# Kernel tuning notes

Hardware: AMD Instinct MI355X
Metric: run time of the kernel (lower is better)

## Reference

```python
import jax, jax.numpy as jnp
import numpy as np

N_NODES = 100000
N_EDGES = 1600000
IN_FEATS = 256
DIMS = [IN_FEATS, 128, 64, 16, 40]


def setup_inputs() -> dict:
    key = jax.random.key(0)
    ks = jax.random.split(key, 3 + 2 * 4)
    x = jax.random.normal(ks[0], (N_NODES, IN_FEATS), dtype=jnp.float32)
    src = jax.random.randint(ks[1], (N_EDGES,), 0, N_NODES)
    dst = jax.random.randint(ks[2], (N_EDGES,), 0, N_NODES)
    inp = {"x": x, "src": src, "dst": dst}
    for i in range(4):
        fan_in = DIMS[i]
        inp[f"W{i+1}"] = jax.random.normal(ks[3 + 2 * i], (DIMS[i], DIMS[i + 1]), dtype=jnp.float32) / np.sqrt(fan_in)
        inp[f"b{i+1}"] = jnp.zeros((DIMS[i + 1],), dtype=jnp.float32)
    return inp


def reference(x, src, dst, W1, b1, W2, b2, W3, b3, W4, b4):
    n = x.shape[0]
    ones = jnp.ones(src.shape[0], dtype=x.dtype)
    # symmetric GCN normalization (DGL norm='both'); clamp deg>=1 like DGL
    deg_out = jnp.maximum(jax.ops.segment_sum(ones, src, num_segments=n), 1.0)
    deg_in = jnp.maximum(jax.ops.segment_sum(ones, dst, num_segments=n), 1.0)
    norm_src = jax.lax.rsqrt(deg_out)[:, None]  # [N,1]
    norm_dst = jax.lax.rsqrt(deg_in)[:, None]   # [N,1]

    def gconv(h, W, b, act):
        # project first (in_feats >= out_feats for every layer, matching DGL ordering)
        h = (h * norm_src) @ W                                   # [N, d_out]
        h = jax.ops.segment_sum(h[src], dst, num_segments=n)      # SpMM aggregate
        h = h * norm_dst + b
        return jax.nn.relu(h) if act else h

    h = gconv(x, W1, b1, True)
    h = gconv(h, W2, b2, True)
    h = gconv(h, W3, b3, True)
    h = gconv(h, W4, b4, False)
    return h
```

## Files before the change

### kernel.cpp

```cpp
#include <hip/hip_runtime.h>


typedef unsigned short ushort_t;

__device__ __forceinline__ void gload_lds16(const float4* g, float4* l) {
    __builtin_amdgcn_global_load_lds(
        (const __attribute__((address_space(1))) void*)g,
        (__attribute__((address_space(3))) void*)l, 16, 0, 0);
}

__device__ __forceinline__ ushort_t f2bf(float f) {
    unsigned u = __float_as_uint(f);
    u += 0x7FFFu + ((u >> 16) & 1u);
    return (ushort_t)(u >> 16);
}
#define BFLO(u) __uint_as_float((u) << 16)
#define BFHI(u) __uint_as_float((u) & 0xffff0000u)

template<int DIN, int DOUT, int RB, int KT, typename EPI>
__device__ __forceinline__ void proj_body(
        const float* __restrict__ in, const float* __restrict__ W,
        int N, int n0, float4* __restrict__ wlds, float4* __restrict__ xlds,
        EPI&& epi) {
    constexpr int CG  = DOUT / 4;
    constexpr int RPP = 256 / CG;
    constexpr int R4  = RB / RPP;
    constexpr int K4T = KT / 4;
    constexpr int NKT = DIN / KT;
    constexpr int XTILE = RB * K4T;
    constexpr int WTILE = KT * CG;
    static_assert(RPP * CG == 256, "full block");
    static_assert((K4T & (K4T - 1)) == 0, "pow2 swizzle");
    static_assert(XTILE % 256 == 0 && WTILE % 256 == 0, "stage granularity");

    const int tid  = threadIdx.x;
    const int wave = tid >> 6;
    const int lane = tid & 63;
    const int rp   = tid / CG;
    const int cg   = tid - rp * CG;

    float4 acc[R4];
#pragma unroll
    for (int r = 0; r < R4; ++r) acc[r] = make_float4(0.f, 0.f, 0.f, 0.f);

    for (int kt = 0; kt < NKT; ++kt) {
        const float4* wsrc = (const float4*)(W + (size_t)kt * KT * DOUT);
#pragma unroll
        for (int j = 0; j < WTILE / 256; ++j) {
            int base = j * 256 + wave * 64;
            gload_lds16(wsrc + base + lane, &wlds[base]);
        }
#pragma unroll
        for (int j = 0; j < XTILE / 256; ++j) {
            int base = j * 256 + wave * 64;
            int fi   = base + lane;
            int row  = fi / K4T;
            int k4   = fi - row * K4T;
            int k4s  = k4 ^ (row & (K4T - 1));
            int grow = n0 + row; if (grow >= N) grow = N - 1;
            const float4* gsrc = (const float4*)(in + (size_t)grow * DIN) + kt * K4T + k4s;
            gload_lds16(gsrc, &xlds[base]);
        }
        __syncthreads();
#pragma unroll 2
        for (int k4 = 0; k4 < K4T; ++k4) {
            float4 w0 = wlds[(k4 * 4 + 0) * CG + cg];
            float4 w1 = wlds[(k4 * 4 + 1) * CG + cg];
            float4 w2 = wlds[(k4 * 4 + 2) * CG + cg];
            float4 w3 = wlds[(k4 * 4 + 3) * CG + cg];
#pragma unroll
            for (int r = 0; r < R4; ++r) {
                int row = rp + r * RPP;
                float4 xv = xlds[row * K4T + (k4 ^ (row & (K4T - 1)))];
                acc[r].x = fmaf(xv.x, w0.x, acc[r].x);
                acc[r].y = fmaf(xv.x, w0.y, acc[r].y);
                acc[r].z = fmaf(xv.x, w0.z, acc[r].z);
                acc[r].w = fmaf(xv.x, w0.w, acc[r].w);
                acc[r].x = fmaf(xv.y, w1.x, acc[r].x);
                acc[r].y = fmaf(xv.y, w1.y, acc[r].y);
                acc[r].z = fmaf(xv.y, w1.z, acc[r].z);
                acc[r].w = fmaf(xv.y, w1.w, acc[r].w);
                acc[r].x = fmaf(xv.z, w2.x, acc[r].x);
                acc[r].y = fmaf(xv.z, w2.y, acc[r].y);
                acc[r].z = fmaf(xv.z, w2.z, acc[r].z);
                acc[r].w = fmaf(xv.z, w2.w, acc[r].w);
                acc[r].x = fmaf(xv.w, w3.x, acc[r].x);
                acc[r].y = fmaf(xv.w, w3.y, acc[r].y);
                acc[r].z = fmaf(xv.w, w3.z, acc[r].z);
                acc[r].w = fmaf(xv.w, w3.w, acc[r].w);
            }
        }
        __syncthreads();
    }
    epi(acc, rp, cg);
}

template<int DIN, int DOUT, int RB, int KT>
__global__ void __launch_bounds__(256) k_comb(
        const float* __restrict__ x, const float* __restrict__ W,
        ushort_t* __restrict__ outbf, int N,
        const int* __restrict__ src, const int* __restrict__ dst,
        int* __restrict__ degO, int* __restrict__ degI,
        int* __restrict__ rank, int E, int PB, int HTH) {
    constexpr int CG  = DOUT / 4;
    constexpr int RPP = 256 / CG;
    constexpr int R4  = RB / RPP;
    constexpr int K4T = KT / 4;
    __shared__ float4 wlds[KT * CG];
    __shared__ float4 xlds[RB * K4T];

    int bid = blockIdx.x, g = bid / 5, r = bid - g * 5;
    if (r == 4) {
        int H = HTH;
        int i = g * 256 + (int)threadIdx.x;
        for (; i + 3 * H < E; i += 4 * H) {
            int s0 = src[i],         d0 = dst[i];
            int s1 = src[i + H],     d1 = dst[i + H];
            int s2 = src[i + 2 * H], d2 = dst[i + 2 * H];
            int s3 = src[i + 3 * H], d3 = dst[i + 3 * H];
            atomicAdd(&degO[s0], 1); atomicAdd(&degO[s1], 1);
            atomicAdd(&degO[s2], 1); atomicAdd(&degO[s3], 1);
            int r0 = atomicAdd(&degI[d0], 1);
            int r1 = atomicAdd(&degI[d1], 1);
            int r2 = atomicAdd(&degI[d2], 1);
            int r3 = atomicAdd(&degI[d3], 1);
            rank[i] = r0; rank[i + H] = r1;
            rank[i + 2 * H] = r2; rank[i + 3 * H] = r3;
        }
        for (; i < E; i += H) {
            atomicAdd(&degO[src[i]], 1);
            rank[i] = atomicAdd(&degI[dst[i]], 1);
        }
        return;
    }
    int pidx = g * 4 + r;
    if (pidx >= PB) return;
    int n0 = pidx * RB;
    proj_body<DIN, DOUT, RB, KT>(x, W, N, n0, wlds, xlds,
        [&](float4 (&acc)[R4], int rp, int cg) {
#pragma unroll
            for (int rr = 0; rr < R4; ++rr) {
                int n = n0 + rp + rr * RPP;
                if (n < N) {
                    ushort4 s;
                    s.x = f2bf(acc[rr].x); s.y = f2bf(acc[rr].y);
                    s.z = f2bf(acc[rr].z); s.w = f2bf(acc[rr].w);
                    *(ushort4*)(outbf + (size_t)n * DOUT + cg * 4) = s;
                }
            }
        });
}

template<int DIN, int DOUT, int RB, int KT>
__global__ void __launch_bounds__(256) k_proj_gl2b(
        const float* __restrict__ in, const float* __restrict__ nrm,
        const float* __restrict__ W, ushort_t* __restrict__ outbf, int N) {
    constexpr int CG  = DOUT / 4;
    constexpr int RPP = 256 / CG;
    constexpr int R4  = RB / RPP;
    constexpr int K4T = KT / 4;
    __shared__ float4 wlds[KT * CG];
    __shared__ float4 xlds[RB * K4T];
    int n0 = blockIdx.x * RB;
    proj_body<DIN, DOUT, RB, KT>(in, W, N, n0, wlds, xlds,
        [&](float4 (&acc)[R4], int rp, int cg) {
#pragma unroll
            for (int rr = 0; rr < R4; ++rr) {
                int n = n0 + rp + rr * RPP;
                if (n < N) {
                    float nm = nrm[n];
                    ushort4 s;
                    s.x = f2bf(acc[rr].x * nm); s.y = f2bf(acc[rr].y * nm);
                    s.z = f2bf(acc[rr].z * nm); s.w = f2bf(acc[rr].w * nm);
                    *(ushort4*)(outbf + (size_t)n * DOUT + cg * 4) = s;
                }
            }
        });
}

__global__ void k_blocksum(const int* __restrict__ degI, const int* __restrict__ degO,
                           int* __restrict__ bsum, float* __restrict__ nSf,
                           float* __restrict__ nDf, int N) {
    __shared__ int sh[256];
    int base = blockIdx.x * 1024;
    int s = 0;
    for (int i = threadIdx.x; i < 1024; i += 256) {
        int idx = base + i;
        if (idx < N) {
            int d = degI[idx];
            s += d;
            nDf[idx] = rsqrtf((float)(d > 1 ? d : 1));
            int a = degO[idx];
            nSf[idx] = rsqrtf((float)(a > 1 ? a : 1));
        }
    }
    sh[threadIdx.x] = s; __syncthreads();
    for (int off = 128; off > 0; off >>= 1) {
        if (threadIdx.x < off) sh[threadIdx.x] += sh[threadIdx.x + off];
        __syncthreads();
    }
    if (threadIdx.x == 0) bsum[blockIdx.x] = sh[0];
}

__global__ void k_blockscan(const int* __restrict__ deg, const int* __restrict__ bsum,
                            int* __restrict__ rowptr, int N, int nb) {
    __shared__ int sh[256];
    int t = threadIdx.x;
    sh[t] = (t < nb) ? bsum[t] : 0;
    __syncthreads();
    for (int off = 1; off < 256; off <<= 1) {
        int v = (t >= off) ? sh[t - off] : 0;
        __syncthreads();
        sh[t] += v;
        __syncthreads();
    }
    int boff = (blockIdx.x > 0) ? sh[blockIdx.x - 1] : 0;
    __syncthreads();
    int base = blockIdx.x * 1024;
    int i0 = base + t * 4;
    int v[4]; int tot = 0;
#pragma unroll
    for (int r = 0; r < 4; ++r) {
        int idx = i0 + r;
        v[r] = (idx < N) ? deg[idx] : 0;
        tot += v[r];
    }
    sh[t] = tot; __syncthreads();
    for (int off = 1; off < 256; off <<= 1) {
        int x = (t >= off) ? sh[t - off] : 0;
        __syncthreads();
        sh[t] += x;
        __syncthreads();
    }
    int run = sh[t] - tot + boff;
#pragma unroll
    for (int r = 0; r < 4; ++r) {
        int idx = i0 + r;
        if (idx < N) rowptr[idx] = run;
        run += v[r];
    }
}

__global__ void k_fill3(const int* __restrict__ src, const int* __restrict__ dst,
                        const int* __restrict__ rank, const int* __restrict__ rowptr,
                        int* __restrict__ col, int E) {
    int stride = gridDim.x * blockDim.x;
    for (int i = blockIdx.x * blockDim.x + threadIdx.x; i < E; i += stride) {
        col[rowptr[dst[i]] + rank[i]] = src[i];
    }
}

__global__ void __launch_bounds__(256) k_gather_l1(
        const int* __restrict__ rowptr, const int* __restrict__ col,
        const int* __restrict__ degI, const float* __restrict__ nSf,
        const float* __restrict__ nDf, const ushort_t* __restrict__ projbf,
        const float* __restrict__ bias, float* __restrict__ out, int N) {
    constexpr int DOUT = 128;
    constexpr int CGB = DOUT / 8;
    long t = blockIdx.x * 256L + threadIdx.x;
    if (t >= (long)N * CGB) return;
    int n  = (int)(t / CGB);
    int cb = (int)(t - (long)n * CGB);
    int beg = rowptr[n];
    int dg  = degI[n];
    float acc[8];
#pragma unroll
    for (int k = 0; k < 8; ++k) acc[k] = 0.f;
    int i = 0;
    for (; i + 4 <= dg; i += 4) {
        int s0 = col[beg + i],     s1 = col[beg + i + 1];
        int s2 = col[beg + i + 2], s3 = col[beg + i + 3];
        uint4 v0 = *(const uint4*)(projbf + (size_t)s0 * DOUT + cb * 8);
        uint4 v1 = *(const uint4*)(projbf + (size_t)s1 * DOUT + cb * 8);
        uint4 v2 = *(const uint4*)(projbf + (size_t)s2 * DOUT + cb * 8);
        uint4 v3 = *(const uint4*)(projbf + (size_t)s3 * DOUT + cb * 8);
        float n0 = nSf[s0], n1 = nSf[s1], n2 = nSf[s2], n3 = nSf[s3];
        acc[0] = fmaf(n0, BFLO(v0.x), fmaf(n1, BFLO(v1.x), fmaf(n2, BFLO(v2.x), fmaf(n3, BFLO(v3.x), acc[0]))));
        acc[1] = fmaf(n0, BFHI(v0.x), fmaf(n1, BFHI(v1.x), fmaf(n2, BFHI(v2.x), fmaf(n3, BFHI(v3.x), acc[1]))));
        acc[2] = fmaf(n0, BFLO(v0.y), fmaf(n1, BFLO(v1.y), fmaf(n2, BFLO(v2.y), fmaf(n3, BFLO(v3.y), acc[2]))));
        acc[3] = fmaf(n0, BFHI(v0.y), fmaf(n1, BFHI(v1.y), fmaf(n2, BFHI(v2.y), fmaf(n3, BFHI(v3.y), acc[3]))));
        acc[4] = fmaf(n0, BFLO(v0.z), fmaf(n1, BFLO(v1.z), fmaf(n2, BFLO(v2.z), fmaf(n3, BFLO(v3.z), acc[4]))));
        acc[5] = fmaf(n0, BFHI(v0.z), fmaf(n1, BFHI(v1.z), fmaf(n2, BFHI(v2.z), fmaf(n3, BFHI(v3.z), acc[5]))));
        acc[6] = fmaf(n0, BFLO(v0.w), fmaf(n1, BFLO(v1.w), fmaf(n2, BFLO(v2.w), fmaf(n3, BFLO(v3.w), acc[6]))));
        acc[7] = fmaf(n0, BFHI(v0.w), fmaf(n1, BFHI(v1.w), fmaf(n2, BFHI(v2.w), fmaf(n3, BFHI(v3.w), acc[7]))));
    }
    for (; i < dg; ++i) {
        int s0 = col[beg + i];
        uint4 v0 = *(const uint4*)(projbf + (size_t)s0 * DOUT + cb * 8);
        float ns0 = nSf[s0];
        acc[0] = fmaf(ns0, BFLO(v0.x), acc[0]);
        acc[1] = fmaf(ns0, BFHI(v0.x), acc[1]);
        acc[2] = fmaf(ns0, BFLO(v0.y), acc[2]);
        acc[3] = fmaf(ns0, BFHI(v0.y), acc[3]);
        acc[4] = fmaf(ns0, BFLO(v0.z), acc[4]);
        acc[5] = fmaf(ns0, BFHI(v0.z), acc[5]);
        acc[6] = fmaf(ns0, BFLO(v0.w), acc[6]);
        acc[7] = fmaf(ns0, BFHI(v0.w), acc[7]);
    }
    float nm = nDf[n];
    const float* bp = bias + cb * 8;
    float o[8];
#pragma unroll
    for (int k = 0; k < 8; ++k) o[k] = fmaxf(fmaf(acc[k], nm, bp[k]), 0.f);
    float* dstp = out + (size_t)n * DOUT + cb * 8;
    *(float4*)(dstp)     = make_float4(o[0], o[1], o[2], o[3]);
    *(float4*)(dstp + 4) = make_float4(o[4], o[5], o[6], o[7]);
}

__global__ void __launch_bounds__(256) k_gather_fuse2(
        const int* __restrict__ rowptr, const int* __restrict__ col,
        const int* __restrict__ degI, const float* __restrict__ nSf,
        const float* __restrict__ nDf, const ushort_t* __restrict__ p2bf,
        const float* __restrict__ b2, const float* __restrict__ W3,
        float* __restrict__ P3, int N) {
    constexpr int DOUT = 64;
    __shared__ float w3s[64 * 16];
    ((float4*)w3s)[threadIdx.x] = ((const float4*)W3)[threadIdx.x];
    __syncthreads();

    long t = blockIdx.x * 256L + threadIdx.x;
    int n = (int)(t >> 3);
    bool valid = n < N;
    if (!valid) n = N - 1;
    int cb = (int)(t & 7);
    int lane = threadIdx.x & 63;
    int gb = lane & ~7;

    int beg = rowptr[n];
    int dg  = degI[n];
    float acc[8];
#pragma unroll
    for (int k = 0; k < 8; ++k) acc[k] = 0.f;
    int i = 0;
    for (; i + 4 <= dg; i += 4) {
        int s0 = col[beg + i],     s1 = col[beg + i + 1];
        int s2 = col[beg + i + 2], s3 = col[beg + i + 3];
        uint4 v0 = *(const uint4*)(p2bf + (size_t)s0 * DOUT + cb * 8);
        uint4 v1 = *(const uint4*)(p2bf + (size_t)s1 * DOUT + cb * 8);
        uint4 v2 = *(const uint4*)(p2bf + (size_t)s2 * DOUT + cb * 8);
        uint4 v3 = *(const uint4*)(p2bf + (size_t)s3 * DOUT + cb * 8);
        acc[0] += BFLO(v0.x) + BFLO(v1.x) + BFLO(v2.x) + BFLO(v3.x);
        acc[1] += BFHI(v0.x) + BFHI(v1.x) + BFHI(v2.x) + BFHI(v3.x);
        acc[2] += BFLO(v0.y) + BFLO(v1.y) + BFLO(v2.y) + BFLO(v3.y);
        acc[3] += BFHI(v0.y) + BFHI(v1.y) + BFHI(v2.y) + BFHI(v3.y);
        acc[4] += BFLO(v0.z) + BFLO(v1.z) + BFLO(v2.z) + BFLO(v3.z);
        acc[5] += BFHI(v0.z) + BFHI(v1.z) + BFHI(v2.z) + BFHI(v3.z);
        acc[6] += BFLO(v0.w) + BFLO(v1.w) + BFLO(v2.w) + BFLO(v3.w);
        acc[7] += BFHI(v0.w) + BFHI(v1.w) + BFHI(v2.w) + BFHI(v3.w);
    }
    for (; i < dg; ++i) {
        int s0 = col[beg + i];
        uint4 v0 = *(const uint4*)(p2bf + (size_t)s0 * DOUT + cb * 8);
        acc[0] += BFLO(v0.x); acc[1] += BFHI(v0.x);
        acc[2] += BFLO(v0.y); acc[3] += BFHI(v0.y);
        acc[4] += BFLO(v0.z); acc[5] += BFHI(v0.z);
        acc[6] += BFLO(v0.w); acc[7] += BFHI(v0.w);
    }
    float nm = nDf[n];
    float ns = nSf[n];
    const float* bp = b2 + cb * 8;
    float o[8];
#pragma unroll
    for (int k = 0; k < 8; ++k)
        o[k] = fmaxf(fmaf(acc[k], nm, bp[k]), 0.f) * ns;
    float y0 = 0.f, y1 = 0.f;
#pragma unroll
    for (int k = 0; k < 64; ++k) {
        float v = __shfl(o[k & 7], gb + (k >> 3), 64);
        y0 = fmaf(v, w3s[k * 16 + 2 * cb], y0);
        y1 = fmaf(v, w3s[k * 16 + 2 * cb + 1], y1);
    }
    if (valid) *(float2*)(P3 + (size_t)n * 16 + 2 * cb) = make_float2(y0, y1);
}

__global__ void __launch_bounds__(256) k_gather_l3(
        const int* __restrict__ rowptr, const int* __restrict__ col,
        const int* __restrict__ degI, const float* __restrict__ nSf,
        const float* __restrict__ nDf, const float* __restrict__ proj,
        const float* __restrict__ bias, float* __restrict__ out, int N) {
    long t = blockIdx.x * 256L + threadIdx.x;
    if (t >= (long)N * 4) return;
    int n  = (int)(t >> 2);
    int cg = (int)(t & 3);
    int beg = rowptr[n];
    int dg  = degI[n];
    float4 a0 = make_float4(0.f, 0.f, 0.f, 0.f);
    float4 a1 = make_float4(0.f, 0.f, 0.f, 0.f);
    float4 a2 = make_float4(0.f, 0.f, 0.f, 0.f);
    float4 a3 = make_float4(0.f, 0.f, 0.f, 0.f);
    int i = 0;
    for (; i + 4 <= dg; i += 4) {
        int s0 = col[beg + i],     s1 = col[beg + i + 1];
        int s2 = col[beg + i + 2], s3 = col[beg + i + 3];
        float4 v0 = *(const float4*)(proj + (size_t)s0 * 16 + cg * 4);
        float4 v1 = *(const float4*)(proj + (size_t)s1 * 16 + cg * 4);
        float4 v2 = *(const float4*)(proj + (size_t)s2 * 16 + cg * 4);
        float4 v3 = *(const float4*)(proj + (size_t)s3 * 16 + cg * 4);
        a0.x += v0.x; a0.y += v0.y; a0.z += v0.z; a0.w += v0.w;
        a1.x += v1.x; a1.y += v1.y; a1.z += v1.z; a1.w += v1.w;
        a2.x += v2.x; a2.y += v2.y; a2.z += v2.z; a2.w += v2.w;
        a3.x += v3.x; a3.y += v3.y; a3.z += v3.z; a3.w += v3.w;
    }
    for (; i < dg; ++i) {
        int s0 = col[beg + i];
        float4 v0 = *(const float4*)(proj + (size_t)s0 * 16 + cg * 4);
        a0.x += v0.x; a0.y += v0.y; a0.z += v0.z; a0.w += v0.w;
    }
    float4 s = make_float4(a0.x + a1.x + a2.x + a3.x, a0.y + a1.y + a2.y + a3.y,
                           a0.z + a1.z + a2.z + a3.z, a0.w + a1.w + a2.w + a3.w);
    float nm = nDf[n];
    float ns = nSf[n];
    float4 b = *(const float4*)(bias + cg * 4);
    float4 o;
    o.x = fmaxf(fmaf(s.x, nm, b.x), 0.f) * ns;
    o.y = fmaxf(fmaf(s.y, nm, b.y), 0.f) * ns;
    o.z = fmaxf(fmaf(s.z, nm, b.z), 0.f) * ns;
    o.w = fmaxf(fmaf(s.w, nm, b.w), 0.f) * ns;
    *(float4*)(out + (size_t)n * 16 + cg * 4) = o;
}

__global__ void __launch_bounds__(256) k_gather_fuse4(
        const int* __restrict__ rowptr, const int* __restrict__ col,
        const int* __restrict__ degI, const float* __restrict__ nDf,
        const float* __restrict__ t4, const float* __restrict__ W4,
        const float* __restrict__ b4, float* __restrict__ out, int N) {
    __shared__ float w4s[16 * 40];
    __shared__ float b4s[40];
    for (int i = threadIdx.x; i < 160; i += 256)
        ((float4*)w4s)[i] = ((const float4*)W4)[i];
    if (threadIdx.x < 40) b4s[threadIdx.x] = b4[threadIdx.x];
    __syncthreads();

    long t = blockIdx.x * 256L + threadIdx.x;
    int n = (int)(t >> 2);
    bool valid = n < N;
    if (!valid) n = N - 1;
    int cg = (int)(t & 3);
    int lane = threadIdx.x & 63;
    int gb = lane & ~3;

    int beg = rowptr[n];
    int dg  = degI[n];
    float4 a0 = make_float4(0.f, 0.f, 0.f, 0.f);
    float4 a1 = make_float4(0.f, 0.f, 0.f, 0.f);
    int i = 0;
    for (; i + 2 <= dg; i += 2) {
        int s0 = col[beg + i], s1 = col[beg + i + 1];
        float4 v0 = *(const float4*)(t4 + (size_t)s0 * 16 + cg * 4);
        float4 v1 = *(const float4*)(t4 + (size_t)s1 * 16 + cg * 4);
        a0.x += v0.x; a0.y += v0.y; a0.z += v0.z; a0.w += v0.w;
        a1.x += v1.x; a1.y += v1.y; a1.z += v1.z; a1.w += v1.w;
    }
    if (i < dg) {
        int s0 = col[beg + i];
        float4 v0 = *(const float4*)(t4 + (size_t)s0 * 16 + cg * 4);
        a0.x += v0.x; a0.y += v0.y; a0.z += v0.z; a0.w += v0.w;
    }
    float av[4] = { a0.x + a1.x, a0.y + a1.y, a0.z + a1.z, a0.w + a1.w };

    float y[10];
#pragma unroll
    for (int jj = 0; jj < 10; ++jj) y[jj] = 0.f;
#pragma unroll
    for (int k = 0; k < 16; ++k) {
        float v = __shfl(av[k & 3], gb + (k >> 2), 64);
        const float* wr = w4s + k * 40 + cg * 10;
#pragma unroll
        for (int jj = 0; jj < 10; ++jj) y[jj] = fmaf(v, wr[jj], y[jj]);
    }
    if (valid) {
        float nm = nDf[n];
        float* dp = out + (size_t)n * 40 + cg * 10;
        const float* bp = b4s + cg * 10;
#pragma unroll
        for (int jj = 0; jj < 10; ++jj) dp[jj] = fmaf(y[jj], nm, bp[jj]);
    }
}

static inline int cdiv(long a, int b) { return (int)((a + b - 1) / b); }

extern "C" void kernel_launch(void* const* d_in, const int* in_sizes, int n_in,
                              void* d_out, int out_size, void* d_ws, size_t ws_size,
                              hipStream_t stream) {
    const float* x   = (const float*)d_in[0];
    const int*   src = (const int*)d_in[1];
    const int*   dst = (const int*)d_in[2];
    const float* W1 = (const float*)d_in[3];  const float* b1 = (const float*)d_in[4];
    const float* W2 = (const float*)d_in[5];  const float* b2 = (const float*)d_in[6];
    const float* W3 = (const float*)d_in[7];  const float* b3 = (const float*)d_in[8];
    const float* W4 = (const float*)d_in[9];  const float* b4 = (const float*)d_in[10];

    const int N = in_sizes[0] / 256;
    const int E = in_sizes[1];

    int* ws_i = (int*)d_ws;
    int* degO   = ws_i;
    int* degI   = ws_i + N;
    int* rowptr = ws_i + 2 * (size_t)N;
    int* col    = ws_i + 3 * (size_t)N;
    int* rank   = ws_i + 3 * (size_t)N + E;
    float* nSf  = (float*)(ws_i + 3 * (size_t)N + 2 * (size_t)E);
    float* nDf  = nSf + N;
    float* projb = nDf + N;
    float* hbuf  = projb + (size_t)N * 64;
    ushort_t* projbf = (ushort_t*)projb;
    float* P3 = projb + (size_t)N * 32;
    int* bsum   = (int*)hbuf;

    int nb = (N + 1023) / 1024;
    int PB = cdiv(N, 64);
    int G5 = cdiv(PB, 4);
    int HTH = G5 * 256;

    hipMemsetAsync(degO, 0, 2 * (size_t)N * sizeof(int), stream);
    k_comb<256, 128, 64, 32><<<5 * G5, 256, 0, stream>>>(
        x, W1, projbf, N, src, dst, degO, degI, rank, E, PB, HTH);

    k_blocksum<<<nb, 256, 0, stream>>>(degI, degO, bsum, nSf, nDf, N);
    k_blockscan<<<nb, 256, 0, stream>>>(degI, bsum, rowptr, N, nb);
    k_fill3<<<2048, 256, 0, stream>>>(src, dst, rank, rowptr, col, E);

    k_gather_l1<<<cdiv((long)N * 16, 256), 256, 0, stream>>>(
        rowptr, col, degI, nSf, nDf, projbf, b1, hbuf, N);

    k_proj_gl2b<128, 64, 64, 32><<<cdiv(N, 64), 256, 0, stream>>>(
        hbuf, nSf, W2, projbf, N);
    k_gather_fuse2<<<cdiv((long)N * 8, 256), 256, 0, stream>>>(
        rowptr, col, degI, nSf, nDf, projbf, b2, W3, P3, N);

    k_gather_l3<<<cdiv((long)N * 4, 256), 256, 0, stream>>>(
        rowptr, col, degI, nSf, nDf, P3, b3, hbuf, N);

    k_gather_fuse4<<<cdiv((long)N * 4, 256), 256, 0, stream>>>(
        rowptr, col, degI, nDf, hbuf, W4, b4, (float*)d_out, N);
}
```

Measured before the change: 380.3 us.

## Store layer-1 activations as bf16 and add bf16-input layer-2 projection kernel

The layer-1 gather now writes its ReLU output as packed bf16 instead of fp32. A new dedicated layer-2 projection kernel reads those bf16 rows through a swizzled LDS tile and unpacks them before the FMA loop. This halves the bytes written and re-read for the intermediate activation, at the cost of extra precision loss in layer-1 outputs. The degree/rank atomic loop in the combined kernel is also simplified to a plain strided loop without the 4x manual unroll.

```diff
diff --git a/kernel.cpp b/kernel.cpp
--- a/kernel.cpp
+++ b/kernel.cpp
@@ -13,6 +13,9 @@
     unsigned u = __float_as_uint(f);
     u += 0x7FFFu + ((u >> 16) & 1u);
     return (ushort_t)(u >> 16);
+}
+__device__ __forceinline__ unsigned pack2bf(float a, float b) {
+    return (unsigned)f2bf(a) | ((unsigned)f2bf(b) << 16);
 }
 #define BFLO(u) __uint_as_float((u) << 16)
 #define BFHI(u) __uint_as_float((u) & 0xffff0000u)
@@ -111,23 +114,8 @@
 
     int bid = blockIdx.x, g = bid / 5, r = bid - g * 5;
     if (r == 4) {
-        int H = HTH;
         int i = g * 256 + (int)threadIdx.x;
-        for (; i + 3 * H < E; i += 4 * H) {
-            int s0 = src[i],         d0 = dst[i];
-            int s1 = src[i + H],     d1 = dst[i + H];
-            int s2 = src[i + 2 * H], d2 = dst[i + 2 * H];
-            int s3 = src[i + 3 * H], d3 = dst[i + 3 * H];
-            atomicAdd(&degO[s0], 1); atomicAdd(&degO[s1], 1);
-            atomicAdd(&degO[s2], 1); atomicAdd(&degO[s3], 1);
-            int r0 = atomicAdd(&degI[d0], 1);
-            int r1 = atomicAdd(&degI[d1], 1);
-            int r2 = atomicAdd(&degI[d2], 1);
-            int r3 = atomicAdd(&degI[d3], 1);
-            rank[i] = r0; rank[i + H] = r1;
-            rank[i + 2 * H] = r2; rank[i + 3 * H] = r3;
-        }
-        for (; i < E; i += H) {
+        for (; i < E; i += HTH) {
             atomicAdd(&degO[src[i]], 1);
             rank[i] = atomicAdd(&degI[dst[i]], 1);
         }
@@ -151,31 +139,64 @@
         });
 }
 
-template<int DIN, int DOUT, int RB, int KT>
-__global__ void __launch_bounds__(256) k_proj_gl2b(
-        const float* __restrict__ in, const float* __restrict__ nrm,
+__global__ void __launch_bounds__(256) k_proj_l2bf(
+        const ushort_t* __restrict__ in, const float* __restrict__ nrm,
         const float* __restrict__ W, ushort_t* __restrict__ outbf, int N) {
-    constexpr int CG  = DOUT / 4;
-    constexpr int RPP = 256 / CG;
-    constexpr int R4  = RB / RPP;
-    constexpr int K4T = KT / 4;
-    __shared__ float4 wlds[KT * CG];
-    __shared__ float4 xlds[RB * K4T];
-    int n0 = blockIdx.x * RB;
-    proj_body<DIN, DOUT, RB, KT>(in, W, N, n0, wlds, xlds,
-        [&](float4 (&acc)[R4], int rp, int cg) {
-#pragma unroll
-            for (int rr = 0; rr < R4; ++rr) {
-                int n = n0 + rp + rr * RPP;
-                if (n < N) {
-                    float nm = nrm[n];
-                    ushort4 s;
-                    s.x = f2bf(acc[rr].x * nm); s.y = f2bf(acc[rr].y * nm);
-                    s.z = f2bf(acc[rr].z * nm); s.w = f2bf(acc[rr].w * nm);
-                    *(ushort4*)(outbf + (size_t)n * DOUT + cg * 4) = s;
+    __shared__ float4 wlds[32 * 16];
+    __shared__ uint4  xlds[64 * 4];
+    const int tid = threadIdx.x;
+    const int rp = tid >> 4, cg = tid & 15;
+    int n0 = blockIdx.x * 64;
+
+    float4 acc[4];
+#pragma unroll
+    for (int r = 0; r < 4; ++r) acc[r] = make_float4(0.f, 0.f, 0.f, 0.f);
+
+    for (int kt = 0; kt < 4; ++kt) {
+        const float4* wsrc = (const float4*)(W + (size_t)kt * 32 * 64);
+        gload_lds16(wsrc + tid, &wlds[tid]);
+        gload_lds16(wsrc + 256 + tid, &wlds[256 + tid]);
+        {
+            int row = tid >> 2, c = tid & 3;
+            int cs = c ^ (row & 3);
+            int grow = n0 + row; if (grow >= N) grow = N - 1;
+            const uint4* gsrc = (const uint4*)(in + (size_t)grow * 128) + kt * 4 + cs;
+            gload_lds16((const float4*)gsrc, (float4*)&xlds[tid]);
+        }
+        __syncthreads();
+#pragma unroll
+        for (int k8 = 0; k8 < 4; ++k8) {
+            float4 w[8];
+#pragma unroll
+            for (int j = 0; j < 8; ++j) w[j] = wlds[(k8 * 8 + j) * 16 + cg];
+#pragma unroll
+            for (int r = 0; r < 4; ++r) {
+                int row = rp + r * 16;
+                uint4 xv = xlds[row * 4 + (k8 ^ (row & 3))];
+                float xf[8] = { BFLO(xv.x), BFHI(xv.x), BFLO(xv.y), BFHI(xv.y),
+                                BFLO(xv.z), BFHI(xv.z), BFLO(xv.w), BFHI(xv.w) };
+#pragma unroll
+                for (int j = 0; j < 8; ++j) {
+                    acc[r].x = fmaf(xf[j], w[j].x, acc[r].x);
+                    acc[r].y = fmaf(xf[j], w[j].y, acc[r].y);
+                    acc[r].z = fmaf(xf[j], w[j].z, acc[r].z);
+                    acc[r].w = fmaf(xf[j], w[j].w, acc[r].w);
                 }
             }
-        });
+        }
+        __syncthreads();
+    }
+#pragma unroll
+    for (int r = 0; r < 4; ++r) {
+        int n = n0 + rp + r * 16;
+        if (n < N) {
+            float nm = nrm[n];
+            ushort4 s;
+            s.x = f2bf(acc[r].x * nm); s.y = f2bf(acc[r].y * nm);
+            s.z = f2bf(acc[r].z * nm); s.w = f2bf(acc[r].w * nm);
+            *(ushort4*)(outbf + (size_t)n * 64 + cg * 4) = s;
+        }
+    }
 }
 
 __global__ void k_blocksum(const int* __restrict__ degI, const int* __restrict__ degO,
@@ -254,7 +275,7 @@
         const int* __restrict__ rowptr, const int* __restrict__ col,
         const int* __restrict__ degI, const float* __restrict__ nSf,
         const float* __restrict__ nDf, const ushort_t* __restrict__ projbf,
-        const float* __restrict__ bias, float* __restrict__ out, int N) {
+        const float* __restrict__ bias, ushort_t* __restrict__ outbf, int N) {
     constexpr int DOUT = 128;
     constexpr int CGB = DOUT / 8;
     long t = blockIdx.x * 256L + threadIdx.x;
@@ -302,9 +323,10 @@
     float o[8];
 #pragma unroll
     for (int k = 0; k < 8; ++k) o[k] = fmaxf(fmaf(acc[k], nm, bp[k]), 0.f);
-    float* dstp = out + (size_t)n * DOUT + cb * 8;
-    *(float4*)(dstp)     = make_float4(o[0], o[1], o[2], o[3]);
-    *(float4*)(dstp + 4) = make_float4(o[4], o[5], o[6], o[7]);
+    uint4 s;
+    s.x = pack2bf(o[0], o[1]); s.y = pack2bf(o[2], o[3]);
+    s.z = pack2bf(o[4], o[5]); s.w = pack2bf(o[6], o[7]);
+    *(uint4*)(outbf + (size_t)n * DOUT + cb * 8) = s;
 }
 
 __global__ void __launch_bounds__(256) k_gather_fuse2(
@@ -504,6 +526,7 @@
     float* projb = nDf + N;
     float* hbuf  = projb + (size_t)N * 64;
     ushort_t* projbf = (ushort_t*)projb;
+    ushort_t* h1bf   = (ushort_t*)hbuf;
     float* P3 = projb + (size_t)N * 32;
     int* bsum   = (int*)hbuf;
 
@@ -521,10 +544,9 @@
     k_fill3<<<2048, 256, 0, stream>>>(src, dst, rank, rowptr, col, E);
 
     k_gather_l1<<<cdiv((long)N * 16, 256), 256, 0, stream>>>(
-        rowptr, col, degI, nSf, nDf, projbf, b1, hbuf, N);
-
-    k_proj_gl2b<128, 64, 64, 32><<<cdiv(N, 64), 256, 0, stream>>>(
-        hbuf, nSf, W2, projbf, N);
+        rowptr, col, degI, nSf, nDf, projbf, b1, h1bf, N);
+
+    k_proj_l2bf<<<cdiv(N, 64), 256, 0, stream>>>(h1bf, nSf, W2, projbf, N);
     k_gather_fuse2<<<cdiv((long)N * 8, 256), 256, 0, stream>>>(
         rowptr, col, degI, nSf, nDf, projbf, b2, W3, P3, N);
 
```

New measurement: 365.4 us. -3.9%, faster.
